# Performance work log

Measured on AMD Instinct MI355X. Metric: run time of the kernel, lower is better.

## Reference

```python
import jax, jax.numpy as jnp
import numpy as np

N, E, G = 100000, 1600000, 8
IN, H, OUT = 3, 64, 20


def setup_inputs() -> dict:
    key = jax.random.key(0)
    ks = jax.random.split(key, 24)
    def nrm(k, shape, scale=0.1):
        return jax.random.normal(k, shape, dtype=jnp.float32) * scale
    inp = {}
    inp["x"] = jax.random.normal(ks[0], (N, IN), dtype=jnp.float32)
    inp["edge_index"] = jax.random.randint(ks[1], (2, E), 0, N, dtype=jnp.int32)
    inp["batch"] = jnp.sort(jax.random.randint(ks[2], (N,), 0, G, dtype=jnp.int32))
    dims = [(IN, H), (H, H), (H, H)]  # 3 GATConv layers (initial + layers-1)
    for i, (di, do) in enumerate(dims):
        inp[f"W{i}"] = nrm(ks[3 + 4 * i], (di, do))
        inp[f"as{i}"] = nrm(ks[4 + 4 * i], (do,))
        inp[f"ad{i}"] = nrm(ks[5 + 4 * i], (do,))
        inp[f"b{i}"] = jnp.zeros((do,), jnp.float32)
    inp["vn_emb0"] = jnp.zeros((1, H), jnp.float32)  # constant-0 init per module
    inp["m1_w1"] = nrm(ks[15], (H, H)); inp["m1_b1"] = jnp.zeros((H,), jnp.float32)
    inp["m1_w2"] = nrm(ks[16], (H, H)); inp["m1_b2"] = jnp.zeros((H,), jnp.float32)
    inp["mf_w1"] = nrm(ks[17], (H, H)); inp["mf_b1"] = jnp.zeros((H,), jnp.float32)
    inp["mf_w2"] = nrm(ks[18], (H, OUT)); inp["mf_b2"] = jnp.zeros((OUT,), jnp.float32)
    inp["out_w"] = nrm(ks[19], (H, OUT)); inp["out_b"] = jnp.zeros((OUT,), jnp.float32)
    return inp


def _gat(x, src, dst, W, a_s, a_d, b):
    # PyG GATConv, 1 head: h = xW; e_ij = LeakyReLU_0.2(a_s.h_j + a_d.h_i);
    # alpha = softmax over incoming edges of each dst node; out_i = sum_j alpha_ij h_j + b
    h = x @ W                                                  # [N, H]
    lg = jax.nn.leaky_relu((h @ a_s)[src] + (h @ a_d)[dst], 0.2)  # [E+N]
    m = jax.ops.segment_max(lg, dst, num_segments=N)
    m = jnp.where(jnp.isfinite(m), m, 0.0)
    p = jnp.exp(lg - m[dst])
    denom = jax.ops.segment_sum(p, dst, num_segments=N)
    alpha = p / denom[dst]
    return jax.ops.segment_sum(alpha[:, None] * h[src], dst, num_segments=N) + b


def _forward(x, edge_index, batch, params):
    (W0, as0, ad0, b0, W1, as1, ad1, b1, W2, as2, ad2, b2,
     vn_emb0, m1_w1, m1_b1, m1_w2, m1_b2, mf_w1, mf_b1, mf_w2, mf_b2,
     out_w, out_b) = params
    loops = jnp.arange(N, dtype=edge_index.dtype)  # GATConv add_self_loops=True
    src = jnp.concatenate([edge_index[0], loops])
    dst = jnp.concatenate([edge_index[1], loops])
    act = lambda v: jax.nn.leaky_relu(v, 0.01)  # nn.LeakyReLU default slope
    h = act(_gat(x, src, dst, W0, as0, ad0, b0))
    h = act(_gat(h, src, dst, W1, as1, ad1, b1))
    h = act(_gat(h, src, dst, W2, as2, ad2, b2))
    # virtual node: global_add_pool(out, batch) + Embedding(0) (zero-init)
    vn = jax.ops.segment_sum(h, batch, num_segments=G) + vn_emb0[0]
    vn = jax.nn.relu(vn @ m1_w1 + m1_b1)
    vn = jax.nn.relu(vn @ m1_w2 + m1_b2)
    vn = jax.nn.relu(vn @ mf_w1 + mf_b1)
    vn = jax.nn.relu(vn @ mf_w2 + mf_b2)
    return (h @ out_w + out_b, vn)


def reference(x, edge_index, batch, W0, as0, ad0, b0, W1, as1, ad1, b1,
              W2, as2, ad2, b2, vn_emb0, m1_w1, m1_b1, m1_w2, m1_b2,
              mf_w1, mf_b1, mf_w2, mf_b2, out_w, out_b):
    params = (W0, as0, ad0, b0, W1, as1, ad1, b1, W2, as2, ad2, b2,
              vn_emb0, m1_w1, m1_b1, m1_w2, m1_b2, mf_w1, mf_b1, mf_w2, mf_b2,
              out_w, out_b)
    return _forward(x, edge_index, batch, params)
```

## Files before the change

### kernel.cpp

```cpp
#include <hip/hip_runtime.h>
#include <hip/hip_bf16.h>

#define H 64
#define OUTD 20
#define NGRAPH 8
#define CAP 64
#define NB 128

typedef __attribute__((ext_vector_type(8))) short bf16x8;
typedef __attribute__((ext_vector_type(4))) float f32x4;

__device__ __forceinline__ float ldp(const void* p, int i, bool f32) {
    return f32 ? ((const float*)p)[i]
               : __bfloat162float(((const __hip_bfloat16*)p)[i]);
}

__device__ __forceinline__ float bfu(unsigned short u) {
    union { unsigned int i; float f; } c; c.i = ((unsigned)u) << 16; return c.f;
}
__device__ __forceinline__ unsigned short fbits(float f) {
    __hip_bfloat16 b = __float2bfloat16(f);
    return *reinterpret_cast<unsigned short*>(&b);
}

__global__ void detect_dtype(const unsigned short* __restrict__ xb, int n_u16,
                             int* __restrict__ flag) {
    __shared__ int sh[256];
    int t = threadIdx.x;
    int m = min(n_u16, 4096);
    int bad = 0;
    for (int i = t; i < m; i += 256) {
        unsigned e = (xb[i] >> 7) & 0xFF;
        bad += (e >= 0x90) ? 1 : 0;
    }
    sh[t] = bad;
    __syncthreads();
    for (int off = 128; off; off >>= 1) {
        if (t < off) sh[t] += sh[t + off];
        __syncthreads();
    }
    if (t == 0) *flag = (sh[0] > (m >> 4)) ? 1 : 0;
}


__global__ void bucketA_dense0(const int* __restrict__ dst, int* __restrict__ bcnt,
                               int E, int n, int nA, int EPC,
                               const void* __restrict__ x, const void* __restrict__ W,
                               const void* __restrict__ a_s, const void* __restrict__ a_d,
                               __hip_bfloat16* __restrict__ h, float* __restrict__ s,
                               float* __restrict__ d, const int* __restrict__ flagp) {
    if ((int)blockIdx.x < nA) {
        __shared__ unsigned acnt[NB];
        int t = threadIdx.x;
        for (int i = t; i < NB; i += 256) acnt[i] = 0;
        __syncthreads();
        int base = blockIdx.x * (256 * EPC) + t;
        for (int i = 0; i < EPC; ++i) {
            int e = base + i * 256;
            if (e < E) {
                int dn = dst[e];
                if ((unsigned)dn < (unsigned)n) atomicAdd(&acnt[dn >> 10], 1u);
            }
        }
        __syncthreads();
        for (int i = t; i < NB; i += 256) bcnt[blockIdx.x * NB + i] = acnt[i];
        return;
    }
    const bool f32 = (*flagp != 0);
    int idx = ((int)blockIdx.x - nA) * 256 + threadIdx.x;
    int node = idx >> 6;
    int f = idx & 63;
    if (node >= n) return;
    float acc = 0.f;
    for (int k = 0; k < 3; ++k)
        acc += ldp(x, node * 3 + k, f32) * ldp(W, k * H + f, f32);
    h[(size_t)node * H + f] = __float2bfloat16(acc);
    float sv = acc * ldp(a_s, f, f32);
    float dv = acc * ldp(a_d, f, f32);
    for (int off = 32; off; off >>= 1) {
        sv += __shfl_xor(sv, off);
        dv += __shfl_xor(dv, off);
    }
    if (f == 0) { s[node] = sv; d[node] = dv; }
}

__global__ void bucketB1(const int* __restrict__ bcnt, int* __restrict__ boff,
                         int* __restrict__ btot, int nA) {
    __shared__ int sh[256];
    int b = blockIdx.x, t = threadIdx.x;
    int v = (t < nA) ? bcnt[t * NB + b] : 0;
    sh[t] = v;
    __syncthreads();
    for (int off = 1; off < 256; off <<= 1) {
        int add = (t >= off) ? sh[t - off] : 0;
        __syncthreads();
        sh[t] += add;
        __syncthreads();
    }
    if (t < nA) boff[t * NB + b] = sh[t] - v;
    if (t == 255) btot[b] = sh[255];
}

__global__ void bucketB2(const int* __restrict__ btot, int* __restrict__ bstart) {
    __shared__ int sh[NB];
    int t = threadIdx.x;
    int v = btot[t];
    sh[t] = v;
    __syncthreads();
    for (int off = 1; off < NB; off <<= 1) {
        int add = (t >= off) ? sh[t - off] : 0;
        __syncthreads();
        sh[t] += add;
        __syncthreads();
    }
    bstart[t] = sh[t] - v;
    if (t == NB - 1) bstart[NB] = sh[NB - 1];
}

__global__ void bucketC(const int* __restrict__ src, const int* __restrict__ dst,
                        const int* __restrict__ boff, const int* __restrict__ bstart,
                        unsigned* __restrict__ ebuf, int E, int n, int EPC) {
    __shared__ int base[NB];
    __shared__ unsigned lcur[NB];
    int t = threadIdx.x;
    for (int i = t; i < NB; i += 256) {
        base[i] = bstart[i] + boff[blockIdx.x * NB + i];
        lcur[i] = 0;
    }
    __syncthreads();
    int eb = blockIdx.x * (256 * EPC) + t;
    for (int i = 0; i < EPC; ++i) {
        int e = eb + i * 256;
        if (e < E) {
            int dn = dst[e];
            if ((unsigned)dn < (unsigned)n) {
                int b = dn >> 10;
                unsigned pos = atomicAdd(&lcur[b], 1u);
                ebuf[base[b] + pos] = ((unsigned)src[e] << 10) | (unsigned)(dn & 1023);
            }
        }
    }
}

__global__ __launch_bounds__(1024) void bucketD(const unsigned* __restrict__ ebuf,
                                                const int* __restrict__ bstart,
                                                int* __restrict__ cnt,
                                                int* __restrict__ col, int n) {
    __shared__ unsigned lcnt[1024];
    int b = blockIdx.x, t = threadIdx.x;
    lcnt[t] = 0;
    __syncthreads();
    int beg = bstart[b], end = bstart[b + 1];
    for (int i = beg + t; i < end; i += 1024) {
        unsigned e = ebuf[i];
        int loc = (int)(e & 1023u);
        int sn = (int)(e >> 10);
        unsigned pos = atomicAdd(&lcnt[loc], 1u);
        if (pos < CAP) col[(size_t)((b << 10) + loc) * CAP + pos] = sn;
    }
    __syncthreads();
    int node = (b << 10) + t;
    if (node < n) cnt[node] = (int)min(lcnt[t], (unsigned)CAP);
}


__global__ __launch_bounds__(256) void denseN_mfma(
    const __hip_bfloat16* __restrict__ in,
    const void* __restrict__ W,
    const void* __restrict__ a_s, const void* __restrict__ a_d,
    __hip_bfloat16* __restrict__ h, float* __restrict__ s,
    float* __restrict__ d, int n, const int* __restrict__ flagp) {
    const bool f32 = (*flagp != 0);
    __shared__ short Wt[64 * 72];
    int t = threadIdx.x;
    for (int i = t; i < 4096; i += 256) {
        int k = i >> 6, nf = i & 63;
        Wt[nf * 72 + k] = (short)fbits(ldp(W, i, f32));
    }
    __syncthreads();

    int wid = t >> 6, lane = t & 63;
    int quad = lane >> 4, n16 = lane & 15;
    int nodeBase = blockIdx.x * 64 + wid * 16;
    int mrow = nodeBase + n16;
    int mclamp = min(mrow, n - 1);
    const short* inp = (const short*)in;
    const short* arow = inp + (size_t)mclamp * 64;
    bf16x8 a0 = *(const bf16x8*)(arow + quad * 8);
    bf16x8 a1 = *(const bf16x8*)(arow + 32 + quad * 8);

    float as_v[4], ad_v[4];
    for (int nt = 0; nt < 4; ++nt) {
        as_v[nt] = ldp(a_s, nt * 16 + n16, f32);
        ad_v[nt] = ldp(a_d, nt * 16 + n16, f32);
    }

    float sv[4] = {0.f, 0.f, 0.f, 0.f}, dv[4] = {0.f, 0.f, 0.f, 0.f};
    f32x4 accs[4];
    for (int nt = 0; nt < 4; ++nt) {
        const short* wrow = Wt + (nt * 16 + n16) * 72;
        bf16x8 b0 = *(const bf16x8*)(wrow + quad * 8);
        bf16x8 b1 = *(const bf16x8*)(wrow + 32 + quad * 8);
        f32x4 c = {0.f, 0.f, 0.f, 0.f};
        c = __builtin_amdgcn_mfma_f32_16x16x32_bf16(a0, b0, c, 0, 0, 0);
        c = __builtin_amdgcn_mfma_f32_16x16x32_bf16(a1, b1, c, 0, 0, 0);
        accs[nt] = c;
        for (int r = 0; r < 4; ++r) {
            sv[r] += c[r] * as_v[nt];
            dv[r] += c[r] * ad_v[nt];
        }
    }

    for (int r = 0; r < 4; ++r) {
        int node = nodeBase + quad * 4 + r;
        if (node < n) {
            __hip_bfloat16* hr = h + (size_t)node * 64;
            for (int nt = 0; nt < 4; ++nt)
                hr[nt * 16 + n16] = __float2bfloat16(accs[nt][r]);
        }
    }
    for (int r = 0; r < 4; ++r) {
        for (int mask = 1; mask < 16; mask <<= 1) {
            sv[r] += __shfl_xor(sv[r], mask);
            dv[r] += __shfl_xor(dv[r], mask);
        }
    }
    if (n16 == 0) {
        for (int r = 0; r < 4; ++r) {
            int node = nodeBase + quad * 4 + r;
            if (node < n) { s[node] = sv[r]; d[node] = dv[r]; }
        }
    }
}


__global__ void gat_aggregate(const __hip_bfloat16* __restrict__ h,
                              const float* __restrict__ s, const float* __restrict__ d,
                              const int* __restrict__ cnt, const int* __restrict__ col,
                              const void* __restrict__ bias,
                              __hip_bfloat16* __restrict__ out, int n,
                              const int* __restrict__ flagp) {
    const bool f32 = (*flagp != 0);
    int node = (blockIdx.x * blockDim.x + threadIdx.x) >> 6;
    if (node >= n) return;
    int lane = threadIdx.x & 63;
    int deg = min(cnt[node], CAP);
    int D = deg + 1;
    size_t base = (size_t)node * CAP;
    float di = d[node];

    if (D <= 64) {
        bool act = lane < D;
        int j = (lane < deg) ? col[base + lane] : node;
        j = ((unsigned)j < (unsigned)n) ? j : 0;
        float v = act ? s[j] + di : -INFINITY;
        v = v > 0.f ? v : 0.2f * v;
        float m = v;
        for (int off = 32; off; off >>= 1) m = fmaxf(m, __shfl_xor(m, off));
        float wgt = act ? __expf(v - m) : 0.f;
        float wsum = wgt;
        for (int off = 32; off; off >>= 1) wsum += __shfl_xor(wsum, off);

        const ushort4* h4 = (const ushort4*)h;
        int c = lane & 15, q = lane >> 4;
        float a0 = 0.f, a1 = 0.f, a2 = 0.f, a3 = 0.f;
        int groups = (D + 3) >> 2;
        for (int p = 0; p < groups; ++p) {
            int t = 4 * p + q;
            float wt = __shfl(wgt, t);
            int jt = __shfl(j, t);
            ushort4 hv = h4[jt * 16 + c];
            a0 += wt * bfu(hv.x);
            a1 += wt * bfu(hv.y);
            a2 += wt * bfu(hv.z);
            a3 += wt * bfu(hv.w);
        }
        a0 += __shfl_xor(a0, 16); a0 += __shfl_xor(a0, 32);
        a1 += __shfl_xor(a1, 16); a1 += __shfl_xor(a1, 32);
        a2 += __shfl_xor(a2, 16); a2 += __shfl_xor(a2, 32);
        a3 += __shfl_xor(a3, 16); a3 += __shfl_xor(a3, 32);
        if (lane < 16) {
            float inv = 1.f / fmaxf(wsum, 1e-20f);
            float o0 = a0 * inv + ldp(bias, 4 * c + 0, f32);
            float o1 = a1 * inv + ldp(bias, 4 * c + 1, f32);
            float o2 = a2 * inv + ldp(bias, 4 * c + 2, f32);
            float o3 = a3 * inv + ldp(bias, 4 * c + 3, f32);
            o0 = o0 > 0.f ? o0 : 0.01f * o0;
            o1 = o1 > 0.f ? o1 : 0.01f * o1;
            o2 = o2 > 0.f ? o2 : 0.01f * o2;
            o3 = o3 > 0.f ? o3 : 0.01f * o3;
            ushort4 ov;
            ov.x = fbits(o0); ov.y = fbits(o1); ov.z = fbits(o2); ov.w = fbits(o3);
            ((ushort4*)out)[(size_t)node * 16 + c] = ov;
        }
        return;
    }

    float m = -INFINITY;
    for (int e = lane; e < D; e += 64) {
        int j = (e < deg) ? col[base + e] : node;
        j = ((unsigned)j < (unsigned)n) ? j : 0;
        float v = s[j] + di;
        v = v > 0.f ? v : 0.2f * v;
        m = fmaxf(m, v);
    }
    for (int off = 32; off; off >>= 1) m = fmaxf(m, __shfl_xor(m, off));
    if (!(m > -INFINITY)) m = 0.f;

    float acc = 0.f, wsum = 0.f;
    for (int b = 0; b < D; b += 64) {
        int e = b + lane;
        float w = 0.f;
        int j = 0;
        if (e < D) {
            j = (e < deg) ? col[base + e] : node;
            j = ((unsigned)j < (unsigned)n) ? j : 0;
            float v = s[j] + di;
            v = v > 0.f ? v : 0.2f * v;
            w = __expf(v - m);
        }
        wsum += w;
        int c2 = min(64, D - b);
        for (int t = 0; t < c2; ++t) {
            float wt = __shfl(w, t);
            int jt = __shfl(j, t);
            acc += wt * __bfloat162float(h[(size_t)jt * H + lane]);
        }
    }
    for (int off = 32; off; off >>= 1) wsum += __shfl_xor(wsum, off);

    float o = acc / fmaxf(wsum, 1e-20f) + ldp(bias, lane, f32);
    o = o > 0.f ? o : 0.01f * o;
    out[(size_t)node * H + lane] = __float2bfloat16(o);
}


__global__ void proj_pool(const __hip_bfloat16* __restrict__ h,
                          const void* __restrict__ W, const void* __restrict__ b,
                          void* __restrict__ out, int n, const int* __restrict__ flagp,
                          int projBlocks, const int* __restrict__ batch,
                          float* __restrict__ vn) {
    if ((int)blockIdx.x < projBlocks) {
        const bool f32 = (*flagp != 0);
        int idx = blockIdx.x * 256 + threadIdx.x;
        if (idx >= n * OUTD) return;
        int node = idx / OUTD;
        int o = idx - node * OUTD;
        float acc = ldp(b, o, f32);
        const __hip_bfloat16* row = h + (size_t)node * H;
        for (int k = 0; k < H; ++k)
            acc += __bfloat162float(row[k]) * ldp(W, k * OUTD + o, f32);
        if (f32) ((float*)out)[idx] = acc;
        else     ((__hip_bfloat16*)out)[idx] = __float2bfloat16(acc);
        return;
    }
    __shared__ float part[NGRAPH * H];
    int t = threadIdx.x;
    for (int i = t; i < NGRAPH * H; i += 256) part[i] = 0.f;
    __syncthreads();
    int pb = (int)blockIdx.x - projBlocks;
    int npb = gridDim.x - projBlocks;
    int wid = t >> 6, lane = t & 63;
    int gwave = pb * 4 + wid;
    int nwaves = npb * 4;
    int chunk = (n + nwaves - 1) / nwaves;
    int beg = gwave * chunk;
    int end = min(n, beg + chunk);
    if (beg < end) {
        float acc = 0.f;
        int cur = batch[beg];
        for (int i = beg; i < end; ++i) {
            int g = batch[i];
            if (g != cur) {
                if ((unsigned)cur < NGRAPH) atomicAdd(&part[cur * H + lane], acc);
                acc = 0.f;
                cur = g;
            }
            acc += __bfloat162float(h[(size_t)i * H + lane]);
        }
        if ((unsigned)cur < NGRAPH) atomicAdd(&part[cur * H + lane], acc);
    }
    __syncthreads();
    for (int i = t; i < NGRAPH * H; i += 256) {
        float v = part[i];
        if (v != 0.f) atomicAdd(&vn[i], v);
    }
}


__global__ void vn_mlp(const float* __restrict__ vn, const void* __restrict__ emb,
                       const void* __restrict__ w1, const void* __restrict__ b1,
                       const void* __restrict__ w2, const void* __restrict__ b2,
                       const void* __restrict__ w3, const void* __restrict__ b3,
                       const void* __restrict__ w4, const void* __restrict__ b4,
                       void* __restrict__ out, int out1_off, const int* __restrict__ flagp) {
    const bool f32 = (*flagp != 0);
    __shared__ float A[NGRAPH * H], B[NGRAPH * H];
    int t = threadIdx.x;
    int g = t >> 6, f = t & 63;
    A[t] = vn[t] + ldp(emb, f, f32);
    __syncthreads();
    float acc = ldp(b1, f, f32);
    for (int k = 0; k < H; ++k) acc += A[g * H + k] * ldp(w1, k * H + f, f32);
    B[t] = fmaxf(acc, 0.f);
    __syncthreads();
    acc = ldp(b2, f, f32);
    for (int k = 0; k < H; ++k) acc += B[g * H + k] * ldp(w2, k * H + f, f32);
    A[t] = fmaxf(acc, 0.f);
    __syncthreads();
    acc = ldp(b3, f, f32);
    for (int k = 0; k < H; ++k) acc += A[g * H + k] * ldp(w3, k * H + f, f32);
    B[t] = fmaxf(acc, 0.f);
    __syncthreads();
    if (f < OUTD) {
        acc = ldp(b4, f, f32);
        for (int k = 0; k < H; ++k) acc += B[g * H + k] * ldp(w4, k * OUTD + f, f32);
        acc = fmaxf(acc, 0.f);
        int idx = out1_off + g * OUTD + f;
        if (f32) ((float*)out)[idx] = acc;
        else     ((__hip_bfloat16*)out)[idx] = __float2bfloat16(acc);
    }
}


extern "C" void kernel_launch(void* const* d_in, const int* in_sizes, int n_in,
                              void* d_out, int out_size, void* d_ws, size_t ws_size,
                              hipStream_t stream) {
    const void* x   = d_in[0];
    const int* ei   = (const int*)d_in[1];
    const int* batch= (const int*)d_in[2];
    const void* W0  = d_in[3];
    const void* as0 = d_in[4];
    const void* ad0 = d_in[5];
    const void* b0  = d_in[6];
    const void* W1  = d_in[7];
    const void* as1 = d_in[8];
    const void* ad1 = d_in[9];
    const void* b1  = d_in[10];
    const void* W2  = d_in[11];
    const void* as2 = d_in[12];
    const void* ad2 = d_in[13];
    const void* b2  = d_in[14];
    const void* vne = d_in[15];
    const void* m1w1 = d_in[16];
    const void* m1b1 = d_in[17];
    const void* m1w2 = d_in[18];
    const void* m1b2 = d_in[19];
    const void* mfw1 = d_in[20];
    const void* mfb1 = d_in[21];
    const void* mfw2 = d_in[22];
    const void* mfb2 = d_in[23];
    const void* outw = d_in[24];
    const void* outb = d_in[25];

    const int N = in_sizes[2];
    const int E = in_sizes[1] / 2;
    const int* srcp = ei;
    const int* dstp = ei + E;

    char* w = (char*)d_ws;
    auto alloc = [&](size_t bytes) -> void* {
        void* p = (void*)w;
        w += ((bytes + 255) / 256) * 256;
        return p;
    };
    int*   flag   = (int*)alloc(256);
    int*   bcnt   = (int*)alloc((size_t)256 * NB * 4);
    int*   boff   = (int*)alloc((size_t)256 * NB * 4);
    int*   btot   = (int*)alloc((size_t)NB * 4);
    int*   bstart = (int*)alloc((size_t)(NB + 1) * 4);
    unsigned* ebuf= (unsigned*)alloc((size_t)E * 4);
    int*   cnt    = (int*)alloc((size_t)N * 4);
    int*   col    = (int*)alloc((size_t)N * CAP * 4);
    __hip_bfloat16* featA = (__hip_bfloat16*)alloc((size_t)N * H * 2);
    __hip_bfloat16* featB = (__hip_bfloat16*)alloc((size_t)N * H * 2);
    __hip_bfloat16* hbuf  = (__hip_bfloat16*)alloc((size_t)N * H * 2);
    float* sArr   = (float*)alloc((size_t)N * 4);
    float* dArr   = (float*)alloc((size_t)N * 4);
    float* vn     = (float*)alloc((size_t)NGRAPH * H * 4);

    const int nbN64 = (N * H + 255) / 256;
    const int nb64 = (N + 63) / 64;
    const int projBlocks = (N * OUTD + 255) / 256;
    int EPC = 32;
    int nA = (E + 256 * EPC - 1) / (256 * EPC);
    while (nA > 256) { EPC <<= 1; nA = (E + 256 * EPC - 1) / (256 * EPC); }

    detect_dtype<<<1, 256, 0, stream>>>((const unsigned short*)x, in_sizes[0], flag);

    hipMemsetAsync(vn, 0, (size_t)NGRAPH * H * 4, stream);
    bucketA_dense0<<<nA + nbN64, 256, 0, stream>>>(
        dstp, bcnt, E, N, nA, EPC, x, W0, as0, ad0, hbuf, sArr, dArr, flag);
    bucketB1<<<NB, 256, 0, stream>>>(bcnt, boff, btot, nA);
    bucketB2<<<1, NB, 0, stream>>>(btot, bstart);
    bucketC<<<nA, 256, 0, stream>>>(srcp, dstp, boff, bstart, ebuf, E, N, EPC);
    bucketD<<<NB, 1024, 0, stream>>>(ebuf, bstart, cnt, col, N);

    gat_aggregate<<<nbN64, 256, 0, stream>>>(hbuf, sArr, dArr, cnt, col, b0, featA, N, flag);
    denseN_mfma<<<nb64, 256, 0, stream>>>(featA, W1, as1, ad1, hbuf, sArr, dArr, N, flag);
    gat_aggregate<<<nbN64, 256, 0, stream>>>(hbuf, sArr, dArr, cnt, col, b1, featB, N, flag);
    denseN_mfma<<<nb64, 256, 0, stream>>>(featB, W2, as2, ad2, hbuf, sArr, dArr, N, flag);
    gat_aggregate<<<nbN64, 256, 0, stream>>>(hbuf, sArr, dArr, cnt, col, b2, featA, N, flag);

    proj_pool<<<projBlocks + 512, 256, 0, stream>>>(featA, outw, outb, d_out, N, flag,
                                                    projBlocks, batch, vn);
    vn_mlp<<<1, 512, 0, stream>>>(vn, vne, m1w1, m1b1, m1w2, m1b2, mfw1, mfb1, mfw2, mfb2,
                                  d_out, N * OUTD, flag);
}
```

Measured before the change: 480.3 us.

## Use MFMA for output projection and 16-byte gathers in GAT aggregation

The final output projection now stages the transposed weight matrix in shared memory as bf16 and computes each 64-node tile with 16x16x32 bf16 MFMA instructions, replacing the per-thread scalar dot-product loop that reread the weights from global memory. The GAT aggregation fast path now gathers 8 bf16 values (16 bytes) per lane and handles 8 edges per iteration instead of 4, which halves the loop trip count at the cost of one extra reduction shuffle round per accumulator. Rounding the weights to bf16 for the projection may change numerics when the inputs are fp32.

```diff
diff --git a/kernel.cpp b/kernel.cpp
--- a/kernel.cpp
+++ b/kernel.cpp
@@ -9,6 +9,7 @@
 
 typedef __attribute__((ext_vector_type(8))) short bf16x8;
 typedef __attribute__((ext_vector_type(4))) float f32x4;
+typedef __attribute__((ext_vector_type(8))) unsigned short u16x8;
 
 __device__ __forceinline__ float ldp(const void* p, int i, bool f32) {
     return f32 ? ((const float*)p)[i]
@@ -261,37 +262,38 @@
         float wsum = wgt;
         for (int off = 32; off; off >>= 1) wsum += __shfl_xor(wsum, off);
 
-        const ushort4* h4 = (const ushort4*)h;
-        int c = lane & 15, q = lane >> 4;
-        float a0 = 0.f, a1 = 0.f, a2 = 0.f, a3 = 0.f;
-        int groups = (D + 3) >> 2;
+        const u16x8* h8 = (const u16x8*)h;
+        int c = lane & 7, q = lane >> 3;
+        float a[8] = {0.f, 0.f, 0.f, 0.f, 0.f, 0.f, 0.f, 0.f};
+        int groups = (D + 7) >> 3;
         for (int p = 0; p < groups; ++p) {
-            int t = 4 * p + q;
+            int t = 8 * p + q;
             float wt = __shfl(wgt, t);
             int jt = __shfl(j, t);
-            ushort4 hv = h4[jt * 16 + c];
-            a0 += wt * bfu(hv.x);
-            a1 += wt * bfu(hv.y);
-            a2 += wt * bfu(hv.z);
-            a3 += wt * bfu(hv.w);
-        }
-        a0 += __shfl_xor(a0, 16); a0 += __shfl_xor(a0, 32);
-        a1 += __shfl_xor(a1, 16); a1 += __shfl_xor(a1, 32);
-        a2 += __shfl_xor(a2, 16); a2 += __shfl_xor(a2, 32);
-        a3 += __shfl_xor(a3, 16); a3 += __shfl_xor(a3, 32);
-        if (lane < 16) {
+            u16x8 hv = h8[jt * 8 + c];
+            a[0] += wt * bfu(hv[0]);
+            a[1] += wt * bfu(hv[1]);
+            a[2] += wt * bfu(hv[2]);
+            a[3] += wt * bfu(hv[3]);
+            a[4] += wt * bfu(hv[4]);
+            a[5] += wt * bfu(hv[5]);
+            a[6] += wt * bfu(hv[6]);
+            a[7] += wt * bfu(hv[7]);
+        }
+        for (int i = 0; i < 8; ++i) {
+            a[i] += __shfl_xor(a[i], 8);
+            a[i] += __shfl_xor(a[i], 16);
+            a[i] += __shfl_xor(a[i], 32);
+        }
+        if (lane < 8) {
             float inv = 1.f / fmaxf(wsum, 1e-20f);
-            float o0 = a0 * inv + ldp(bias, 4 * c + 0, f32);
-            float o1 = a1 * inv + ldp(bias, 4 * c + 1, f32);
-            float o2 = a2 * inv + ldp(bias, 4 * c + 2, f32);
-            float o3 = a3 * inv + ldp(bias, 4 * c + 3, f32);
-            o0 = o0 > 0.f ? o0 : 0.01f * o0;
-            o1 = o1 > 0.f ? o1 : 0.01f * o1;
-            o2 = o2 > 0.f ? o2 : 0.01f * o2;
-            o3 = o3 > 0.f ? o3 : 0.01f * o3;
-            ushort4 ov;
-            ov.x = fbits(o0); ov.y = fbits(o1); ov.z = fbits(o2); ov.w = fbits(o3);
-            ((ushort4*)out)[(size_t)node * 16 + c] = ov;
+            u16x8 ov;
+            for (int i = 0; i < 8; ++i) {
+                float o = a[i] * inv + ldp(bias, 8 * c + i, f32);
+                o = o > 0.f ? o : 0.01f * o;
+                ov[i] = fbits(o);
+            }
+            ((u16x8*)out)[(size_t)node * 8 + c] = ov;
         }
         return;
     }
@@ -335,23 +337,58 @@
 }
 
 
-__global__ void proj_pool(const __hip_bfloat16* __restrict__ h,
-                          const void* __restrict__ W, const void* __restrict__ b,
-                          void* __restrict__ out, int n, const int* __restrict__ flagp,
-                          int projBlocks, const int* __restrict__ batch,
-                          float* __restrict__ vn) {
+__global__ __launch_bounds__(256) void proj_pool(
+    const __hip_bfloat16* __restrict__ h,
+    const void* __restrict__ W, const void* __restrict__ b,
+    void* __restrict__ out, int n, const int* __restrict__ flagp,
+    int projBlocks, const int* __restrict__ batch, float* __restrict__ vn) {
+    const bool f32 = (*flagp != 0);
     if ((int)blockIdx.x < projBlocks) {
-        const bool f32 = (*flagp != 0);
-        int idx = blockIdx.x * 256 + threadIdx.x;
-        if (idx >= n * OUTD) return;
-        int node = idx / OUTD;
-        int o = idx - node * OUTD;
-        float acc = ldp(b, o, f32);
-        const __hip_bfloat16* row = h + (size_t)node * H;
-        for (int k = 0; k < H; ++k)
-            acc += __bfloat162float(row[k]) * ldp(W, k * OUTD + o, f32);
-        if (f32) ((float*)out)[idx] = acc;
-        else     ((__hip_bfloat16*)out)[idx] = __float2bfloat16(acc);
+        __shared__ short Wt[32 * 72];
+        int t = threadIdx.x;
+        for (int i = t; i < 32 * 64; i += 256) {
+            int o = i >> 6, k = i & 63;
+            Wt[o * 72 + k] = (o < OUTD) ? (short)fbits(ldp(W, k * OUTD + o, f32)) : 0;
+        }
+        __syncthreads();
+
+        int wid = t >> 6, lane = t & 63;
+        int quad = lane >> 4, n16 = lane & 15;
+        int nodeBase = blockIdx.x * 64 + wid * 16;
+        int mclamp = min(nodeBase + n16, n - 1);
+        const short* arow = (const short*)h + (size_t)mclamp * 64;
+        bf16x8 a0 = *(const bf16x8*)(arow + quad * 8);
+        bf16x8 a1 = *(const bf16x8*)(arow + 32 + quad * 8);
+
+        f32x4 acc0 = {0.f, 0.f, 0.f, 0.f}, acc1 = {0.f, 0.f, 0.f, 0.f};
+        {
+            const short* wrow = Wt + n16 * 72;
+            bf16x8 b0 = *(const bf16x8*)(wrow + quad * 8);
+            bf16x8 b1 = *(const bf16x8*)(wrow + 32 + quad * 8);
+            acc0 = __builtin_amdgcn_mfma_f32_16x16x32_bf16(a0, b0, acc0, 0, 0, 0);
+            acc0 = __builtin_amdgcn_mfma_f32_16x16x32_bf16(a1, b1, acc0, 0, 0, 0);
+        }
+        {
+            const short* wrow = Wt + (16 + n16) * 72;
+            bf16x8 b0 = *(const bf16x8*)(wrow + quad * 8);
+            bf16x8 b1 = *(const bf16x8*)(wrow + 32 + quad * 8);
+            acc1 = __builtin_amdgcn_mfma_f32_16x16x32_bf16(a0, b0, acc1, 0, 0, 0);
+            acc1 = __builtin_amdgcn_mfma_f32_16x16x32_bf16(a1, b1, acc1, 0, 0, 0);
+        }
+        float bv0 = ldp(b, n16, f32);
+        float bv1 = (n16 < OUTD - 16) ? ldp(b, 16 + n16, f32) : 0.f;
+        for (int r = 0; r < 4; ++r) {
+            int node = nodeBase + quad * 4 + r;
+            if (node >= n) break;
+            float o0 = acc0[r] + bv0;
+            if (f32) ((float*)out)[node * OUTD + n16] = o0;
+            else     ((__hip_bfloat16*)out)[node * OUTD + n16] = __float2bfloat16(o0);
+            if (n16 < OUTD - 16) {
+                float o1 = acc1[r] + bv1;
+                if (f32) ((float*)out)[node * OUTD + 16 + n16] = o1;
+                else     ((__hip_bfloat16*)out)[node * OUTD + 16 + n16] = __float2bfloat16(o1);
+            }
+        }
         return;
     }
     __shared__ float part[NGRAPH * H];
@@ -481,7 +518,7 @@
 
     const int nbN64 = (N * H + 255) / 256;
     const int nb64 = (N + 63) / 64;
-    const int projBlocks = (N * OUTD + 255) / 256;
+    const int projBlocks = (N + 63) / 64;
     int EPC = 32;
     int nA = (E + 256 * EPC - 1) / (256 * EPC);
     while (nA > 256) { EPC <<= 1; nA = (E + 256 * EPC - 1) / (256 * EPC); }
```

After: 440.0 us. 8.4% less time.
